# Performance work log

Hardware: AMD Instinct MI355X
Metric: run time of the kernel (lower is better)

The kernel has to match this reference:

```python
import jax, jax.numpy as jnp
import numpy as np

B = 8192
FEAT = 7680
HID = 512
LOC = 4
N_SCENES = 72


def setup_inputs() -> dict:
    key = jax.random.key(0)
    ks = jax.random.split(key, 12)
    s = lambda fan_in: 1.0 / np.sqrt(fan_in)
    inp = {
        "feat": jax.random.normal(ks[0], (B, FEAT), dtype=jnp.float32),
        "scene_idx": jax.random.randint(ks[1], (B,), 0, N_SCENES, dtype=jnp.int64),
        # visual_fc1: Linear(7680 -> 512)  (torch layout: W[out, in])
        "W1": jax.random.uniform(ks[2], (HID, FEAT), jnp.float32, -s(FEAT), s(FEAT)),
        "b1": jax.random.uniform(ks[3], (HID,), jnp.float32, -s(FEAT), s(FEAT)),
        # localization_fc: Linear(512 -> 512), ReLU, Linear(512 -> 4)
        "W2": jax.random.uniform(ks[4], (HID, HID), jnp.float32, -s(HID), s(HID)),
        "b2": jax.random.uniform(ks[5], (HID,), jnp.float32, -s(HID), s(HID)),
        "W3": jax.random.uniform(ks[6], (LOC, HID), jnp.float32, -s(HID), s(HID)),
        "b3": jax.random.uniform(ks[7], (LOC,), jnp.float32, -s(HID), s(HID)),
        # per-scene 2x2 affine (with bias) and 2x2 rotation (no bias)
        "xyW": jax.random.uniform(ks[8], (N_SCENES, 2, 2), jnp.float32, -s(2), s(2)),
        "xyb": jax.random.uniform(ks[9], (N_SCENES, 2), jnp.float32, -s(2), s(2)),
        "tW": jax.random.uniform(ks[10], (N_SCENES, 2, 2), jnp.float32, -s(2), s(2)),
    }
    return inp


def reference(feat, scene_idx, W1, b1, W2, b2, W3, b3, xyW, xyb, tW):
    # visual_fc1: Flatten (already flat) -> Linear -> ReLU
    h = jax.nn.relu(feat @ W1.T + b1)                 # [B, HID]
    # localization_fc: Linear -> ReLU -> Linear
    h = jax.nn.relu(h @ W2.T + b2)                    # [B, HID]
    shared = h @ W3.T + b3                            # [B, 4]
    # per-scene routed 2x2 linears: gather weights per sample, apply, "scatter" is
    # implicit since every row gets exactly one scene's transform.
    sidx = scene_idx.astype(jnp.int32)
    Wxy = xyW[sidx]                                   # [B, 2, 2]
    bxy = xyb[sidx]                                   # [B, 2]
    Wt = tW[sidx]                                     # [B, 2, 2]
    xy = jnp.einsum("boi,bi->bo", Wxy, shared[:, :2]) + bxy
    t = jnp.einsum("boi,bi->bo", Wt, shared[:, 2:])
    return jnp.concatenate([xy, t], axis=1)           # [B, 4]
```

## Files before the change

kernel.cpp:

```cpp
#include <hip/hip_runtime.h>
#include <stdint.h>
#include <stddef.h>

#define BROWS 8192
#define FEATK 7680
#define HIDN  512

typedef __attribute__((ext_vector_type(8))) __bf16 bf16x8;
typedef __attribute__((ext_vector_type(4))) float f32x4;

__device__ __forceinline__ unsigned short f2b(float f) {
  unsigned int u = __float_as_uint(f);
  unsigned int r = (u + 0x7FFFu + ((u >> 16) & 1u)) >> 16;
  return (unsigned short)r;
}

__global__ void cvt_kernel(const float* __restrict__ src, unsigned short* __restrict__ dst, int n4) {
  int i = blockIdx.x * blockDim.x + threadIdx.x;
  int stride = gridDim.x * blockDim.x;
  for (; i < n4; i += stride) {
    float4 v = ((const float4*)src)[i];
    ushort4 o;
    o.x = f2b(v.x); o.y = f2b(v.y); o.z = f2b(v.z); o.w = f2b(v.w);
    ((ushort4*)dst)[i] = o;
  }
}

#define K1_BM 64
#define K1_BK 32

__global__ __launch_bounds__(256, 2) void gemm1_fused_splitk(
    const float* __restrict__ A,
    const unsigned short* __restrict__ Bm,
    float* __restrict__ P,
    int M, int N, int K, int klen) {
  __shared__ unsigned short As[K1_BM * K1_BK];
  __shared__ unsigned short Bs[HIDN * K1_BK];

  const int tid  = threadIdx.x;
  const int lane = tid & 63;
  const int wid  = tid >> 6;
  const int l16  = lane & 15;
  const int quad = lane >> 4;

  const int rowBase = blockIdx.y * K1_BM;
  const int k_begin = blockIdx.x * klen;

  f32x4 acc[4][8] = {};

  for (int k0 = k_begin; k0 < k_begin + klen; k0 += K1_BK) {
#pragma unroll
    for (int it = 0; it < 2; ++it) {
      int c   = it * 256 + tid;
      int row = c >> 3;
      int kq  = c & 7;
      const float4* ga = (const float4*)(A + (size_t)(rowBase + row) * K + k0 + kq * 4);
      float4 v = *ga;
      ushort4 o;
      o.x = f2b(v.x); o.y = f2b(v.y); o.z = f2b(v.z); o.w = f2b(v.w);
      *(ushort4*)(As + row * K1_BK + kq * 4) = o;
    }
#pragma unroll
    for (int it = 0; it < 8; ++it) {
      int cb  = it * 256 + wid * 64;
      int c   = cb + lane;
      int row = c >> 2;
      int kk  = (c & 3) << 3;
      const unsigned short* gb = Bm + (size_t)row * K + (k0 + kk);
      __builtin_amdgcn_global_load_lds(
          (const __attribute__((address_space(1))) void*)gb,
          (__attribute__((address_space(3))) void*)(Bs + (size_t)cb * 8), 16, 0, 0);
    }
    __syncthreads();

    bf16x8 af[4], bfr[8];
#pragma unroll
    for (int mt = 0; mt < 4; ++mt)
      af[mt] = *(const bf16x8*)(As + (mt * 16 + l16) * K1_BK + quad * 8);
#pragma unroll
    for (int nt = 0; nt < 8; ++nt)
      bfr[nt] = *(const bf16x8*)(Bs + (wid * 128 + nt * 16 + l16) * K1_BK + quad * 8);
#pragma unroll
    for (int mt = 0; mt < 4; ++mt)
#pragma unroll
      for (int nt = 0; nt < 8; ++nt)
        acc[mt][nt] = __builtin_amdgcn_mfma_f32_16x16x32_bf16(af[mt], bfr[nt], acc[mt][nt], 0, 0, 0);
    __syncthreads();
  }

  float* outp = P + (size_t)blockIdx.x * M * N;
#pragma unroll
  for (int mt = 0; mt < 4; ++mt) {
#pragma unroll
    for (int r = 0; r < 4; ++r) {
      int row = rowBase + mt * 16 + quad * 4 + r;
      float* cp = outp + (size_t)row * N + wid * 128 + l16;
#pragma unroll
      for (int nt = 0; nt < 8; ++nt) cp[nt * 16] = acc[mt][nt][r];
    }
  }
}

__global__ __launch_bounds__(256) void reduce4_bias_relu(
    const float* __restrict__ P, const float* __restrict__ bias,
    unsigned short* __restrict__ H, int MN4, int N4) {
  int i = blockIdx.x * blockDim.x + threadIdx.x;
  if (i >= MN4) return;
  const float4* p = (const float4*)P;
  float4 a = p[i];
  float4 b = p[i + MN4];
  float4 c = p[i + 2 * MN4];
  float4 d = p[i + 3 * MN4];
  float4 bs = ((const float4*)bias)[i % N4];
  ushort4 o;
  o.x = f2b(fmaxf(a.x + b.x + c.x + d.x + bs.x, 0.0f));
  o.y = f2b(fmaxf(a.y + b.y + c.y + d.y + bs.y, 0.0f));
  o.z = f2b(fmaxf(a.z + b.z + c.z + d.z + bs.z, 0.0f));
  o.w = f2b(fmaxf(a.w + b.w + c.w + d.w + bs.w, 0.0f));
  ((ushort4*)H)[i] = o;
}

#define BM 128
#define BN 128
#define BK 64

__global__ __launch_bounds__(256, 2) void gemm_bt_bias_relu(
    const unsigned short* __restrict__ A,
    const unsigned short* __restrict__ Bm,
    const float* __restrict__ bias,
    unsigned short* __restrict__ C,
    int M, int N, int K) {
  __shared__ unsigned short As[BM * BK];
  __shared__ unsigned short Bs[BN * BK];
  const int tid  = threadIdx.x;
  const int lane = tid & 63;
  const int wid  = tid >> 6;
  const int wm   = wid >> 1;
  const int wn   = wid & 1;
  const int l16  = lane & 15;
  const int quad = lane >> 4;
  const int rowBase = blockIdx.y * BM;
  const int colBase = blockIdx.x * BN;

  f32x4 acc[4][4] = {};

  for (int k0 = 0; k0 < K; k0 += BK) {
#pragma unroll
    for (int it = 0; it < 4; ++it) {
      int cb = it * 256 + wid * 64;
      int c  = cb + lane;
      int row = c >> 3;
      int kk  = (c & 7) << 3;
      const unsigned short* ga = A + (size_t)(rowBase + row) * K + (k0 + kk);
      __builtin_amdgcn_global_load_lds(
          (const __attribute__((address_space(1))) void*)ga,
          (__attribute__((address_space(3))) void*)(As + (size_t)cb * 8), 16, 0, 0);
      const unsigned short* gb = Bm + (size_t)(colBase + row) * K + (k0 + kk);
      __builtin_amdgcn_global_load_lds(
          (const __attribute__((address_space(1))) void*)gb,
          (__attribute__((address_space(3))) void*)(Bs + (size_t)cb * 8), 16, 0, 0);
    }
    __syncthreads();
#pragma unroll
    for (int kk = 0; kk < BK; kk += 32) {
      bf16x8 af[4], bfr[4];
#pragma unroll
      for (int mt = 0; mt < 4; ++mt)
        af[mt] = *(const bf16x8*)(As + (wm * 64 + mt * 16 + l16) * BK + kk + quad * 8);
#pragma unroll
      for (int nt = 0; nt < 4; ++nt)
        bfr[nt] = *(const bf16x8*)(Bs + (wn * 64 + nt * 16 + l16) * BK + kk + quad * 8);
#pragma unroll
      for (int mt = 0; mt < 4; ++mt)
#pragma unroll
        for (int nt = 0; nt < 4; ++nt)
          acc[mt][nt] = __builtin_amdgcn_mfma_f32_16x16x32_bf16(af[mt], bfr[nt], acc[mt][nt], 0, 0, 0);
    }
    __syncthreads();
  }

  float bvals[4];
#pragma unroll
  for (int nt = 0; nt < 4; ++nt) bvals[nt] = bias[colBase + wn * 64 + nt * 16 + l16];
#pragma unroll
  for (int mt = 0; mt < 4; ++mt) {
#pragma unroll
    for (int r = 0; r < 4; ++r) {
      int row = rowBase + wm * 64 + mt * 16 + quad * 4 + r;
      unsigned short* cp = C + (size_t)row * N + colBase + wn * 64 + l16;
#pragma unroll
      for (int nt = 0; nt < 4; ++nt) {
        float v = fmaxf(acc[mt][nt][r] + bvals[nt], 0.0f);
        cp[nt * 16] = f2b(v);
      }
    }
  }
}

__global__ __launch_bounds__(256) void head_kernel(
    const unsigned short* __restrict__ h2,
    const float* __restrict__ W3,
    const float* __restrict__ b3,
    const int* __restrict__ sidx,
    const float* __restrict__ xyW,
    const float* __restrict__ xyb,
    const float* __restrict__ tW,
    float* __restrict__ out) {
  int wave = (blockIdx.x * blockDim.x + threadIdx.x) >> 6;
  int lane = threadIdx.x & 63;
  if (wave >= BROWS) return;

  bf16x8 hv = *(const bf16x8*)(h2 + (size_t)wave * 512 + lane * 8);
  float hf[8];
#pragma unroll
  for (int j = 0; j < 8; ++j) hf[j] = (float)hv[j];

  float s[4];
#pragma unroll
  for (int o = 0; o < 4; ++o) {
    const float* wrow = W3 + o * 512 + lane * 8;
    float4 w0 = ((const float4*)wrow)[0];
    float4 w1 = ((const float4*)wrow)[1];
    float a = hf[0] * w0.x + hf[1] * w0.y + hf[2] * w0.z + hf[3] * w0.w +
              hf[4] * w1.x + hf[5] * w1.y + hf[6] * w1.z + hf[7] * w1.w;
#pragma unroll
    for (int off = 32; off > 0; off >>= 1) a += __shfl_down(a, off, 64);
    s[o] = a;
  }

  if (lane == 0) {
#pragma unroll
    for (int o = 0; o < 4; ++o) s[o] += b3[o];
    int sc = sidx[wave];
    const float* wx = xyW + sc * 4;
    const float* bx = xyb + sc * 2;
    const float* wt = tW + sc * 4;
    float o0 = wx[0] * s[0] + wx[1] * s[1] + bx[0];
    float o1 = wx[2] * s[0] + wx[3] * s[1] + bx[1];
    float o2 = wt[0] * s[2] + wt[1] * s[3];
    float o3 = wt[2] * s[2] + wt[3] * s[3];
    ((float4*)out)[wave] = make_float4(o0, o1, o2, o3);
  }
}

#define WS_W1B   0UL
#define WS_W2B   7864320UL
#define WS_H1    8388608UL
#define WS_H2    16777216UL
#define WS_PART  25165824UL
#define WS_NEED  92274688UL

extern "C" void kernel_launch(void* const* d_in, const int* in_sizes, int n_in,
                              void* d_out, int out_size, void* d_ws, size_t ws_size,
                              hipStream_t stream) {
  const float* feat = (const float*)d_in[0];
  const int*   sidx = (const int*)d_in[1];
  const float* W1   = (const float*)d_in[2];
  const float* b1   = (const float*)d_in[3];
  const float* W2   = (const float*)d_in[4];
  const float* b2   = (const float*)d_in[5];
  const float* W3   = (const float*)d_in[6];
  const float* b3   = (const float*)d_in[7];
  const float* xyW  = (const float*)d_in[8];
  const float* xyb  = (const float*)d_in[9];
  const float* tW   = (const float*)d_in[10];
  float* out = (float*)d_out;

  if (ws_size < WS_NEED) return;

  char* ws = (char*)d_ws;
  unsigned short* W1B  = (unsigned short*)(ws + WS_W1B);
  unsigned short* W2B  = (unsigned short*)(ws + WS_W2B);
  unsigned short* h1   = (unsigned short*)(ws + WS_H1);
  unsigned short* h2   = (unsigned short*)(ws + WS_H2);
  float*          part = (float*)(ws + WS_PART);

  cvt_kernel<<<512, 256, 0, stream>>>(W1, W1B, (HIDN * FEATK) / 4);
  cvt_kernel<<<64, 256, 0, stream>>>(W2, W2B, (HIDN * HIDN) / 4);

  gemm1_fused_splitk<<<dim3(4, BROWS / K1_BM), 256, 0, stream>>>(
      feat, W1B, part, BROWS, HIDN, FEATK, FEATK / 4);
  reduce4_bias_relu<<<(BROWS * HIDN / 4 + 255) / 256, 256, 0, stream>>>(
      part, b1, h1, BROWS * HIDN / 4, HIDN / 4);

  gemm_bt_bias_relu<<<dim3(HIDN / BN, BROWS / BM), 256, 0, stream>>>(
      h1, W2B, b2, h2, BROWS, HIDN, HIDN);

  head_kernel<<<(BROWS * 64) / 256, 256, 0, stream>>>(
      h2, W3, b3, sidx, xyW, xyb, tW, out);
}
```

Baseline: 480.4 us.

## Prefetch next K tile into registers and pad LDS rows in gemm1

The split-K GEMM1 loop now loads the next K tile of A (fp32) and B (bf16) into registers while MFMAs run on the current LDS tile, then converts and stores it to LDS after a barrier. The direct global_load_lds path for B is replaced with register-staged loads. LDS rows are padded from 32 to 40 elements to reduce bank conflicts on fragment reads. This costs extra registers (10 vector loads held across the MFMA block) and an extra barrier per iteration, which may reduce occupancy under the 2-blocks launch bound.

```diff
diff --git a/kernel.cpp b/kernel.cpp
--- a/kernel.cpp
+++ b/kernel.cpp
@@ -26,16 +26,17 @@
   }
 }
 
-#define K1_BM 64
-#define K1_BK 32
+#define K1_BM  64
+#define K1_BK  32
+#define K1_PAD 40
 
 __global__ __launch_bounds__(256, 2) void gemm1_fused_splitk(
     const float* __restrict__ A,
     const unsigned short* __restrict__ Bm,
     float* __restrict__ P,
     int M, int N, int K, int klen) {
-  __shared__ unsigned short As[K1_BM * K1_BK];
-  __shared__ unsigned short Bs[HIDN * K1_BK];
+  __shared__ unsigned short As[K1_BM * K1_PAD];
+  __shared__ unsigned short Bs[HIDN * K1_PAD];
 
   const int tid  = threadIdx.x;
   const int lane = tid & 63;
@@ -45,46 +46,67 @@
 
   const int rowBase = blockIdx.y * K1_BM;
   const int k_begin = blockIdx.x * klen;
+  const int niter   = klen / K1_BK;
 
   f32x4 acc[4][8] = {};
 
-  for (int k0 = k_begin; k0 < k_begin + klen; k0 += K1_BK) {
-#pragma unroll
-    for (int it = 0; it < 2; ++it) {
-      int c   = it * 256 + tid;
-      int row = c >> 3;
-      int kq  = c & 7;
-      const float4* ga = (const float4*)(A + (size_t)(rowBase + row) * K + k0 + kq * 4);
-      float4 v = *ga;
-      ushort4 o;
-      o.x = f2b(v.x); o.y = f2b(v.y); o.z = f2b(v.z); o.w = f2b(v.w);
-      *(ushort4*)(As + row * K1_BK + kq * 4) = o;
-    }
-#pragma unroll
-    for (int it = 0; it < 8; ++it) {
-      int cb  = it * 256 + wid * 64;
-      int c   = cb + lane;
-      int row = c >> 2;
-      int kk  = (c & 3) << 3;
-      const unsigned short* gb = Bm + (size_t)row * K + (k0 + kk);
-      __builtin_amdgcn_global_load_lds(
-          (const __attribute__((address_space(1))) void*)gb,
-          (__attribute__((address_space(3))) void*)(Bs + (size_t)cb * 8), 16, 0, 0);
-    }
-    __syncthreads();
+  float4 aA[2];
+  uint4  bB[8];
+
+#define K1_GLOAD(k0)                                                              \
+  {                                                                               \
+    _Pragma("unroll")                                                             \
+    for (int it = 0; it < 2; ++it) {                                              \
+      int c = it * 256 + tid; int row = c >> 3; int kq = c & 7;                   \
+      aA[it] = *(const float4*)(A + (size_t)(rowBase + row) * K + (k0) + kq * 4); \
+    }                                                                             \
+    _Pragma("unroll")                                                             \
+    for (int it = 0; it < 8; ++it) {                                              \
+      int c = it * 256 + tid; int row = c >> 2; int ch = c & 3;                   \
+      bB[it] = *(const uint4*)(Bm + (size_t)row * K + (k0) + ch * 8);             \
+    }                                                                             \
+  }
+
+#define K1_STORE_LDS()                                                            \
+  {                                                                               \
+    _Pragma("unroll")                                                             \
+    for (int it = 0; it < 2; ++it) {                                              \
+      int c = it * 256 + tid; int row = c >> 3; int kq = c & 7;                   \
+      ushort4 o;                                                                  \
+      o.x = f2b(aA[it].x); o.y = f2b(aA[it].y);                                   \
+      o.z = f2b(aA[it].z); o.w = f2b(aA[it].w);                                   \
+      *(ushort4*)(As + row * K1_PAD + kq * 4) = o;                                \
+    }                                                                             \
+    _Pragma("unroll")                                                             \
+    for (int it = 0; it < 8; ++it) {                                              \
+      int c = it * 256 + tid; int row = c >> 2; int ch = c & 3;                   \
+      *(uint4*)(Bs + row * K1_PAD + ch * 8) = bB[it];                             \
+    }                                                                             \
+  }
+
+  K1_GLOAD(k_begin)
+  K1_STORE_LDS()
+  __syncthreads();
+
+  for (int i = 1; i <= niter; ++i) {
+    const bool more = (i < niter);
+    if (more) K1_GLOAD(k_begin + i * K1_BK)
 
     bf16x8 af[4], bfr[8];
 #pragma unroll
     for (int mt = 0; mt < 4; ++mt)
-      af[mt] = *(const bf16x8*)(As + (mt * 16 + l16) * K1_BK + quad * 8);
+      af[mt] = *(const bf16x8*)(As + (mt * 16 + l16) * K1_PAD + quad * 8);
 #pragma unroll
     for (int nt = 0; nt < 8; ++nt)
-      bfr[nt] = *(const bf16x8*)(Bs + (wid * 128 + nt * 16 + l16) * K1_BK + quad * 8);
+      bfr[nt] = *(const bf16x8*)(Bs + (wid * 128 + nt * 16 + l16) * K1_PAD + quad * 8);
 #pragma unroll
     for (int mt = 0; mt < 4; ++mt)
 #pragma unroll
       for (int nt = 0; nt < 8; ++nt)
         acc[mt][nt] = __builtin_amdgcn_mfma_f32_16x16x32_bf16(af[mt], bfr[nt], acc[mt][nt], 0, 0, 0);
+
+    __syncthreads();
+    if (more) { K1_STORE_LDS() }
     __syncthreads();
   }
 
@@ -99,6 +121,8 @@
       for (int nt = 0; nt < 8; ++nt) cp[nt * 16] = acc[mt][nt][r];
     }
   }
+#undef K1_GLOAD
+#undef K1_STORE_LDS
 }
 
 __global__ __launch_bounds__(256) void reduce4_bias_relu(
```

Result: slower. 658.2 us (+37.0%).

## Replace LDS-staged split-K GEMM1 with direct global-to-register MFMA fragments

Applied to the files above, without the earlier changes.

GEMM1 no longer stages A and B tiles through shared memory. Each lane loads its MFMA fragments straight from global memory, converting fp32 activations to bf16 in registers. The grid now splits N into two 256-column halves and adds a K-split z dimension, with smaller per-wave tiles and higher occupancy hints. This removes the barriers and LDS traffic, but the fp32 feature matrix is read twice and the per-lane row-strided loads may coalesce poorly.

```diff
diff --git a/kernel.cpp b/kernel.cpp
--- a/kernel.cpp
+++ b/kernel.cpp
@@ -26,77 +26,62 @@
   }
 }
 
-#define K1_BM 64
-#define K1_BK 32
-
-__global__ __launch_bounds__(256, 2) void gemm1_fused_splitk(
+__global__ __launch_bounds__(256, 3) void gemm1_direct_splitk(
     const float* __restrict__ A,
     const unsigned short* __restrict__ Bm,
     float* __restrict__ P,
     int M, int N, int K, int klen) {
-  __shared__ unsigned short As[K1_BM * K1_BK];
-  __shared__ unsigned short Bs[HIDN * K1_BK];
-
-  const int tid  = threadIdx.x;
-  const int lane = tid & 63;
-  const int wid  = tid >> 6;
+  const int lane = threadIdx.x & 63;
+  const int wid  = threadIdx.x >> 6;
   const int l16  = lane & 15;
   const int quad = lane >> 4;
 
-  const int rowBase = blockIdx.y * K1_BM;
-  const int k_begin = blockIdx.x * klen;
-
-  f32x4 acc[4][8] = {};
-
-  for (int k0 = k_begin; k0 < k_begin + klen; k0 += K1_BK) {
-#pragma unroll
-    for (int it = 0; it < 2; ++it) {
-      int c   = it * 256 + tid;
-      int row = c >> 3;
-      int kq  = c & 7;
-      const float4* ga = (const float4*)(A + (size_t)(rowBase + row) * K + k0 + kq * 4);
-      float4 v = *ga;
-      ushort4 o;
-      o.x = f2b(v.x); o.y = f2b(v.y); o.z = f2b(v.z); o.w = f2b(v.w);
-      *(ushort4*)(As + row * K1_BK + kq * 4) = o;
-    }
-#pragma unroll
-    for (int it = 0; it < 8; ++it) {
-      int cb  = it * 256 + wid * 64;
-      int c   = cb + lane;
-      int row = c >> 2;
-      int kk  = (c & 3) << 3;
-      const unsigned short* gb = Bm + (size_t)row * K + (k0 + kk);
-      __builtin_amdgcn_global_load_lds(
-          (const __attribute__((address_space(1))) void*)gb,
-          (__attribute__((address_space(3))) void*)(Bs + (size_t)cb * 8), 16, 0, 0);
-    }
-    __syncthreads();
-
-    bf16x8 af[4], bfr[8];
+  const int rowBase = blockIdx.y * 64;
+  const int colBase = blockIdx.x * 256 + wid * 64;
+  const int k_begin = blockIdx.z * klen;
+
+  const float* arow[4];
+#pragma unroll
+  for (int mt = 0; mt < 4; ++mt)
+    arow[mt] = A + (size_t)(rowBase + mt * 16 + l16) * K + quad * 8 + k_begin;
+  const unsigned short* brow[4];
+#pragma unroll
+  for (int nt = 0; nt < 4; ++nt)
+    brow[nt] = Bm + (size_t)(colBase + nt * 16 + l16) * K + quad * 8 + k_begin;
+
+  f32x4 acc[4][4] = {};
+
+#pragma unroll 2
+  for (int k = 0; k < klen; k += 32) {
+    bf16x8 af[4], bfr[4];
+#pragma unroll
+    for (int nt = 0; nt < 4; ++nt)
+      bfr[nt] = *(const bf16x8*)(brow[nt] + k);
+#pragma unroll
+    for (int mt = 0; mt < 4; ++mt) {
+      float4 x = *(const float4*)(arow[mt] + k);
+      float4 y = *(const float4*)(arow[mt] + k + 4);
+      union { bf16x8 v; unsigned short s[8]; } u;
+      u.s[0] = f2b(x.x); u.s[1] = f2b(x.y); u.s[2] = f2b(x.z); u.s[3] = f2b(x.w);
+      u.s[4] = f2b(y.x); u.s[5] = f2b(y.y); u.s[6] = f2b(y.z); u.s[7] = f2b(y.w);
+      af[mt] = u.v;
+    }
 #pragma unroll
     for (int mt = 0; mt < 4; ++mt)
-      af[mt] = *(const bf16x8*)(As + (mt * 16 + l16) * K1_BK + quad * 8);
-#pragma unroll
-    for (int nt = 0; nt < 8; ++nt)
-      bfr[nt] = *(const bf16x8*)(Bs + (wid * 128 + nt * 16 + l16) * K1_BK + quad * 8);
-#pragma unroll
-    for (int mt = 0; mt < 4; ++mt)
-#pragma unroll
-      for (int nt = 0; nt < 8; ++nt)
+#pragma unroll
+      for (int nt = 0; nt < 4; ++nt)
         acc[mt][nt] = __builtin_amdgcn_mfma_f32_16x16x32_bf16(af[mt], bfr[nt], acc[mt][nt], 0, 0, 0);
-    __syncthreads();
-  }
-
-  float* outp = P + (size_t)blockIdx.x * M * N;
+  }
+
+  float* outp = P + (size_t)blockIdx.z * M * N;
 #pragma unroll
   for (int mt = 0; mt < 4; ++mt) {
 #pragma unroll
     for (int r = 0; r < 4; ++r) {
       int row = rowBase + mt * 16 + quad * 4 + r;
-      float* cp = outp + (size_t)row * N + wid * 128 + l16;
-#pragma unroll
-      for (int nt = 0; nt < 8; ++nt) cp[nt * 16] = acc[mt][nt][r];
+      float* cp = outp + (size_t)row * N + colBase + l16;
+#pragma unroll
+      for (int nt = 0; nt < 4; ++nt) cp[nt * 16] = acc[mt][nt][r];
     }
   }
 }
@@ -278,7 +263,7 @@
   cvt_kernel<<<512, 256, 0, stream>>>(W1, W1B, (HIDN * FEATK) / 4);
   cvt_kernel<<<64, 256, 0, stream>>>(W2, W2B, (HIDN * HIDN) / 4);
 
-  gemm1_fused_splitk<<<dim3(4, BROWS / K1_BM), 256, 0, stream>>>(
+  gemm1_direct_splitk<<<dim3(2, BROWS / 64, 4), 256, 0, stream>>>(
       feat, W1B, part, BROWS, HIDN, FEATK, FEATK / 4);
   reduce4_bias_relu<<<(BROWS * HIDN / 4 + 255) / 256, 256, 0, stream>>>(
       part, b1, h1, BROWS * HIDN / 4, HIDN / 4);
```

Result: slower. 704.0 us (+46.6%).
